# Optimization experiments

Measured on AMD Instinct MI355X. Metric: run time of the kernel, lower is better.

## Reference

```python
import jax, jax.numpy as jnp
import numpy as np

N_NODES = 100000
N_EDGES = 625000
D = 128


def setup_inputs() -> dict:
    key = jax.random.key(0)
    ks = jax.random.split(key, 6)
    x = jax.random.normal(ks[0], (N_NODES, D), dtype=jnp.float32)
    src = jax.random.randint(ks[1], (N_EDGES,), 0, N_NODES, dtype=jnp.int32)
    dst = jnp.sort(jax.random.randint(ks[2], (N_EDGES,), 0, N_NODES, dtype=jnp.int32))
    edge_w = jax.random.uniform(ks[3], (N_EDGES,), dtype=jnp.float32)
    # linear layer params (fan-in scaled)
    W = jax.random.normal(ks[4], (D, D), dtype=jnp.float32) / np.sqrt(D)
    b = jnp.zeros((D,), dtype=jnp.float32)
    # highway gate params (glorot-uniform-ish range as in source)
    init_range = np.sqrt(2.0 / (D + D)).astype(np.float32)
    kernel_gate = jax.random.uniform(ks[5], (D, D), dtype=jnp.float32,
                                     minval=-init_range, maxval=init_range)
    bias_gate = jnp.zeros((D,), dtype=jnp.float32)
    return {"x": x, "src": src, "dst": dst, "edge_w": edge_w,
            "W": W, "b": b, "kernel_gate": kernel_gate, "bias_gate": bias_gate}


def reference(x, src, dst, edge_w, W, b, kernel_gate, bias_gate):
    # hidden = Linear(x); dropout is identity in eval mode
    hidden = x @ W.T + b                                  # [N, D]
    # support = spmm(adj, hidden): gather src rows, weight, scatter-add to dst
    msgs = edge_w[:, None] * hidden[src]                  # [E, D]
    support = jax.ops.segment_sum(msgs, dst, num_segments=x.shape[0])
    support = jax.nn.relu(support)                        # act
    # highway gate
    gate = jax.nn.sigmoid(x @ kernel_gate + bias_gate)    # [N, D]
    out = gate * support + (1.0 - gate) * x
    return out
```

## Files before the change

kernel.cpp:

```cpp
#include <hip/hip_runtime.h>

#define DD 128

typedef __attribute__((ext_vector_type(8))) short bf16x8;
typedef __attribute__((ext_vector_type(4))) float f32x4;

__device__ __forceinline__ unsigned int cvt_pk_bf16(float lo, float hi) {
  unsigned int r;
  asm("v_cvt_pk_bf16_f32 %0, %1, %2" : "=v"(r) : "v"(lo), "v"(hi));
  return r;
}
__device__ __forceinline__ float bf_lo(unsigned int v) { return __uint_as_float(v << 16); }
__device__ __forceinline__ float bf_hi(unsigned int v) { return __uint_as_float(v & 0xFFFF0000u); }

__global__ void prep_kernel(const float* __restrict__ x, const int* __restrict__ dst,
                            const float* __restrict__ W, const float* __restrict__ KG,
                            unsigned short* __restrict__ xb, int* __restrict__ row_start,
                            unsigned short* __restrict__ B, int N, int E) {
  int i = blockIdx.x * 256 + threadIdx.x;
  int NC = N * (DD / 4);
  if (i < NC) {
    float4 v = ((const float4*)x)[i];
    uint2 q = {cvt_pk_bf16(v.x, v.y), cvt_pk_bf16(v.z, v.w)};
    ((uint2*)xb)[i] = q;
  } else if (i < NC + E + 1) {
    int e = i - NC;
    if (e == 0) {
      int d0 = dst[0];
      for (int n = 0; n <= d0; ++n) row_start[n] = 0;
    } else if (e == E) {
      for (int n = dst[E - 1] + 1; n <= N; ++n) row_start[n] = E;
    } else {
      int d = dst[e], dp = dst[e - 1];
      for (int n = dp + 1; n <= d; ++n) row_start[n] = e;
    }
  } else if (i < NC + E + 1 + 2 * DD * DD) {
    int e2 = i - (NC + E + 1);
    int j = e2 >> 7, k = e2 & 127;
    float v = (j < DD) ? W[j * DD + k] : KG[k * DD + (j - DD)];
    B[e2] = (unsigned short)cvt_pk_bf16(v, v);
  }
}

__global__ __launch_bounds__(256, 8) void scatter_agg(
    const unsigned short* __restrict__ xb, const int* __restrict__ src,
    const float* __restrict__ ew, const int* __restrict__ row_start,
    unsigned short* __restrict__ aggb, float* __restrict__ sumw, int N, int E) {
  int t = threadIdx.x;
  int wid = t >> 6, lane = t & 63;
  int q = lane >> 4, lr = lane & 15;
  int n = blockIdx.x * 16 + wid * 4 + q;
  bool valid = (n < N);
  int b = valid ? row_start[n] : 0;
  int cnt = valid ? (row_start[n + 1] - b) : 0;
  const uint4* x16 = (const uint4*)xb;

  float a[8];
#pragma unroll
  for (int k = 0; k < 8; ++k) a[k] = 0.f;
  float wsum = 0.f;
  int clampj = cnt > 0 ? cnt - 1 : 0;

  int i = 0;
  while (__any(i < cnt)) {
#pragma unroll
    for (int u = 0; u < 4; ++u) {
      int ii = i + u;
      int jj = ii < clampj ? ii : clampj;
      int j = b + jj;
      if (j > E - 1) j = E - 1;
      float wt = (ii < cnt) ? ew[j] : 0.f;
      int s = src[j];
      uint4 v = x16[(size_t)s * 16 + lr];
      wsum += wt;
      a[0] += wt * bf_lo(v.x); a[1] += wt * bf_hi(v.x);
      a[2] += wt * bf_lo(v.y); a[3] += wt * bf_hi(v.y);
      a[4] += wt * bf_lo(v.z); a[5] += wt * bf_hi(v.z);
      a[6] += wt * bf_lo(v.w); a[7] += wt * bf_hi(v.w);
    }
    i += 4;
  }

  if (valid) {
    uint4 o;
    o.x = cvt_pk_bf16(a[0], a[1]);
    o.y = cvt_pk_bf16(a[2], a[3]);
    o.z = cvt_pk_bf16(a[4], a[5]);
    o.w = cvt_pk_bf16(a[6], a[7]);
    ((uint4*)aggb)[(size_t)n * 16 + lr] = o;
    if (lr == 0) sumw[n] = wsum;
  }
}

__global__ __launch_bounds__(256, 2) void fused_gemm(
    const unsigned short* __restrict__ xb, const unsigned short* __restrict__ aggb,
    const unsigned short* __restrict__ B, const float* __restrict__ sumw,
    const float* __restrict__ bias, const float* __restrict__ bg,
    float* __restrict__ out, int N) {
  __shared__ char smem[32 * 1024];
  unsigned short* sX = (unsigned short*)smem;
  unsigned short* sA = (unsigned short*)(smem + 16384);
  int t = threadIdx.x;
  int wid = t >> 6, lane = t & 63;
  int lr = lane & 15, lk2 = lane >> 4;
  int jw = wid * 32;
  int M0 = blockIdx.x * 64;

  bf16x8 wS[4][2], wG[4][2];
#pragma unroll
  for (int kc = 0; kc < 4; ++kc)
#pragma unroll
    for (int m = 0; m < 2; ++m) {
      int j = jw + m * 16 + lr;
      wS[kc][m] = *(const bf16x8*)(B + (size_t)j * DD + kc * 32 + lk2 * 8);
      wG[kc][m] = *(const bf16x8*)(B + (size_t)(DD + j) * DD + kc * 32 + lk2 * 8);
    }
  float b4[2][4], bg4[2][4];
#pragma unroll
  for (int m = 0; m < 2; ++m) {
    *(float4*)b4[m]  = *(const float4*)&bias[jw + m * 16 + lk2 * 4];
    *(float4*)bg4[m] = *(const float4*)&bg[jw + m * 16 + lk2 * 4];
  }

#pragma unroll
  for (int i = 0; i < 4; ++i) {
    int idx = i * 256 + t;
    int r = idx >> 4, c = idx & 15;
    uint4 vx, va;
    if (M0 + r < N) {
      vx = ((const uint4*)(xb + (size_t)(M0 + r) * DD))[c];
      va = ((const uint4*)(aggb + (size_t)(M0 + r) * DD))[c];
    } else {
      vx = make_uint4(0, 0, 0, 0);
      va = make_uint4(0, 0, 0, 0);
    }
    int off = (r * 256 + c * 16) ^ ((r & 7) << 4);
    *(uint4*)((char*)sX + off) = vx;
    *(uint4*)((char*)sA + off) = va;
  }
  __syncthreads();

  f32x4 accS[2][4], accG[2][4];
#pragma unroll
  for (int m = 0; m < 2; ++m)
#pragma unroll
    for (int nr = 0; nr < 4; ++nr) {
      accS[m][nr] = (f32x4){0.f, 0.f, 0.f, 0.f};
      accG[m][nr] = (f32x4){0.f, 0.f, 0.f, 0.f};
    }

#pragma unroll
  for (int kc = 0; kc < 4; ++kc) {
    int kb = (kc * 32 + lk2 * 8) * 2;
    bf16x8 af[4], xf[4];
#pragma unroll
    for (int nr = 0; nr < 4; ++nr) {
      int r = nr * 16 + lr;
      int off = (r * 256 + kb) ^ ((r & 7) << 4);
      af[nr] = *(const bf16x8*)((const char*)sA + off);
      xf[nr] = *(const bf16x8*)((const char*)sX + off);
    }
#pragma unroll
    for (int m = 0; m < 2; ++m)
#pragma unroll
      for (int nr = 0; nr < 4; ++nr) {
        accS[m][nr] = __builtin_amdgcn_mfma_f32_16x16x32_bf16(wS[kc][m], af[nr], accS[m][nr], 0, 0, 0);
        accG[m][nr] = __builtin_amdgcn_mfma_f32_16x16x32_bf16(wG[kc][m], xf[nr], accG[m][nr], 0, 0, 0);
      }
  }

#pragma unroll
  for (int m = 0; m < 2; ++m) {
    int j0 = jw + m * 16 + lk2 * 4;
#pragma unroll
    for (int nr = 0; nr < 4; ++nr) {
      int node = M0 + nr * 16 + lr;
      if (node < N) {
        float sw = sumw[node];
        int r = nr * 16 + lr;
        uint2 qx = *(const uint2*)((const char*)sX + ((r * 256 + j0 * 2) ^ ((r & 7) << 4)));
        float xr[4] = {bf_lo(qx.x), bf_hi(qx.x), bf_lo(qx.y), bf_hi(qx.y)};
        f32x4 vs = accS[m][nr], vg = accG[m][nr];
        float4 o;
        float* op = &o.x;
#pragma unroll
        for (int reg = 0; reg < 4; ++reg) {
          float s = fmaxf(vs[reg] + sw * b4[m][reg], 0.f);
          float g = 1.0f / (1.0f + __expf(-(vg[reg] + bg4[m][reg])));
          op[reg] = g * s + (1.0f - g) * xr[reg];
        }
        *(float4*)&out[(size_t)node * DD + j0] = o;
      }
    }
  }
}

extern "C" void kernel_launch(void* const* d_in, const int* in_sizes, int n_in,
                              void* d_out, int out_size, void* d_ws, size_t ws_size,
                              hipStream_t stream) {
  const float* x   = (const float*)d_in[0];
  const int*   src = (const int*)d_in[1];
  const int*   dst = (const int*)d_in[2];
  const float* ew  = (const float*)d_in[3];
  const float* W   = (const float*)d_in[4];
  const float* b   = (const float*)d_in[5];
  const float* KG  = (const float*)d_in[6];
  const float* bg  = (const float*)d_in[7];
  float* out = (float*)d_out;

  int N = in_sizes[0] / DD;
  int E = in_sizes[1];

  unsigned short* xbuf = (unsigned short*)d_ws;
  unsigned short* aggb = xbuf + (size_t)N * DD;
  unsigned short* B    = aggb + (size_t)N * DD;
  float* sumw = (float*)(B + 2 * DD * DD);
  int* row_start = (int*)(sumw + N);

  int totalPrep = N * (DD / 4) + (E + 1) + 2 * DD * DD;
  prep_kernel<<<(totalPrep + 255) / 256, 256, 0, stream>>>(x, dst, W, KG, xbuf, row_start, B, N, E);
  scatter_agg<<<(N + 15) / 16, 256, 0, stream>>>(xbuf, src, ew, row_start, aggb, sumw, N, E);
  fused_gemm<<<(N + 63) / 64, 256, 0, stream>>>(xbuf, aggb, B, sumw, b, bg, out, N);
}
```

Baseline: 81.73 us.

## Fuse gather-aggregation into GEMM kernel via shared-memory staging

```diff
diff --git a/kernel.cpp b/kernel.cpp
--- a/kernel.cpp
+++ b/kernel.cpp
@@ -42,101 +42,87 @@
   }
 }
 
-__global__ __launch_bounds__(256, 8) void scatter_agg(
-    const unsigned short* __restrict__ xb, const int* __restrict__ src,
-    const float* __restrict__ ew, const int* __restrict__ row_start,
-    unsigned short* __restrict__ aggb, float* __restrict__ sumw, int N, int E) {
+__global__ __launch_bounds__(256, 2) void mega_kernel(
+    const unsigned short* __restrict__ xb, const unsigned short* __restrict__ B,
+    const int* __restrict__ src, const float* __restrict__ ew,
+    const int* __restrict__ row_start, const float* __restrict__ bias,
+    const float* __restrict__ bg, float* __restrict__ out, int N, int E) {
+  __shared__ char smem[32 * 1024 + 256];
+  unsigned short* sX = (unsigned short*)smem;
+  unsigned short* sA = (unsigned short*)(smem + 16384);
+  float* sumw_s = (float*)(smem + 32768);
   int t = threadIdx.x;
   int wid = t >> 6, lane = t & 63;
-  int q = lane >> 4, lr = lane & 15;
-  int n = blockIdx.x * 16 + wid * 4 + q;
-  bool valid = (n < N);
-  int b = valid ? row_start[n] : 0;
-  int cnt = valid ? (row_start[n + 1] - b) : 0;
+  int lr = lane & 15, lk2 = lane >> 4;
+  int jw = wid * 32;
+  int M0 = blockIdx.x * 64;
+
+  bf16x8 wS[4][2], wG[4][2];
+#pragma unroll
+  for (int kc = 0; kc < 4; ++kc)
+#pragma unroll
+    for (int m = 0; m < 2; ++m) {
+      int j = jw + m * 16 + lr;
+      wS[kc][m] = *(const bf16x8*)(B + (size_t)j * DD + kc * 32 + lk2 * 8);
+      wG[kc][m] = *(const bf16x8*)(B + (size_t)(DD + j) * DD + kc * 32 + lk2 * 8);
+    }
+  float b4[2][4], bg4[2][4];
+#pragma unroll
+  for (int m = 0; m < 2; ++m) {
+    *(float4*)b4[m]  = *(const float4*)&bias[jw + m * 16 + lk2 * 4];
+    *(float4*)bg4[m] = *(const float4*)&bg[jw + m * 16 + lk2 * 4];
+  }
+
+#pragma unroll
+  for (int i = 0; i < 4; ++i) {
+    int idx = i * 256 + t;
+    int r = idx >> 4, c = idx & 15;
+    uint4 vx;
+    if (M0 + r < N) vx = ((const uint4*)(xb + (size_t)(M0 + r) * DD))[c];
+    else            vx = make_uint4(0, 0, 0, 0);
+    int off = (r * 256 + c * 16) ^ ((r & 7) << 4);
+    *(uint4*)((char*)sX + off) = vx;
+  }
+
   const uint4* x16 = (const uint4*)xb;
-
-  float a[8];
-#pragma unroll
-  for (int k = 0; k < 8; ++k) a[k] = 0.f;
-  float wsum = 0.f;
-  int clampj = cnt > 0 ? cnt - 1 : 0;
-
-  int i = 0;
-  while (__any(i < cnt)) {
-#pragma unroll
-    for (int u = 0; u < 4; ++u) {
-      int ii = i + u;
-      int jj = ii < clampj ? ii : clampj;
-      int j = b + jj;
-      if (j > E - 1) j = E - 1;
-      float wt = (ii < cnt) ? ew[j] : 0.f;
-      int s = src[j];
-      uint4 v = x16[(size_t)s * 16 + lr];
-      wsum += wt;
-      a[0] += wt * bf_lo(v.x); a[1] += wt * bf_hi(v.x);
-      a[2] += wt * bf_lo(v.y); a[3] += wt * bf_hi(v.y);
-      a[4] += wt * bf_lo(v.z); a[5] += wt * bf_hi(v.z);
-      a[6] += wt * bf_lo(v.w); a[7] += wt * bf_hi(v.w);
-    }
-    i += 4;
-  }
-
-  if (valid) {
+  for (int p = 0; p < 4; ++p) {
+    int rt = wid * 16 + p * 4 + lk2;
+    int n = M0 + rt;
+    bool valid = (n < N);
+    int b = valid ? row_start[n] : 0;
+    int cnt = valid ? (row_start[n + 1] - b) : 0;
+    float a[8];
+#pragma unroll
+    for (int k = 0; k < 8; ++k) a[k] = 0.f;
+    float wsum = 0.f;
+    int clampj = cnt > 0 ? cnt - 1 : 0;
+    int i = 0;
+    while (__any(i < cnt)) {
+#pragma unroll
+      for (int u = 0; u < 4; ++u) {
+        int ii = i + u;
+        int jj = ii < clampj ? ii : clampj;
+        int j = b + jj;
+        if (j > E - 1) j = E - 1;
+        float wt = (ii < cnt) ? ew[j] : 0.f;
+        int s = src[j];
+        uint4 v = x16[(size_t)s * 16 + lr];
+        wsum += wt;
+        a[0] += wt * bf_lo(v.x); a[1] += wt * bf_hi(v.x);
+        a[2] += wt * bf_lo(v.y); a[3] += wt * bf_hi(v.y);
+        a[4] += wt * bf_lo(v.z); a[5] += wt * bf_hi(v.z);
+        a[6] += wt * bf_lo(v.w); a[7] += wt * bf_hi(v.w);
+      }
+      i += 4;
+    }
     uint4 o;
     o.x = cvt_pk_bf16(a[0], a[1]);
     o.y = cvt_pk_bf16(a[2], a[3]);
     o.z = cvt_pk_bf16(a[4], a[5]);
     o.w = cvt_pk_bf16(a[6], a[7]);
-    ((uint4*)aggb)[(size_t)n * 16 + lr] = o;
-    if (lr == 0) sumw[n] = wsum;
-  }
-}
-
-__global__ __launch_bounds__(256, 2) void fused_gemm(
-    const unsigned short* __restrict__ xb, const unsigned short* __restrict__ aggb,
-    const unsigned short* __restrict__ B, const float* __restrict__ sumw,
-    const float* __restrict__ bias, const float* __restrict__ bg,
-    float* __restrict__ out, int N) {
-  __shared__ char smem[32 * 1024];
-  unsigned short* sX = (unsigned short*)smem;
-  unsigned short* sA = (unsigned short*)(smem + 16384);
-  int t = threadIdx.x;
-  int wid = t >> 6, lane = t & 63;
-  int lr = lane & 15, lk2 = lane >> 4;
-  int jw = wid * 32;
-  int M0 = blockIdx.x * 64;
-
-  bf16x8 wS[4][2], wG[4][2];
-#pragma unroll
-  for (int kc = 0; kc < 4; ++kc)
-#pragma unroll
-    for (int m = 0; m < 2; ++m) {
-      int j = jw + m * 16 + lr;
-      wS[kc][m] = *(const bf16x8*)(B + (size_t)j * DD + kc * 32 + lk2 * 8);
-      wG[kc][m] = *(const bf16x8*)(B + (size_t)(DD + j) * DD + kc * 32 + lk2 * 8);
-    }
-  float b4[2][4], bg4[2][4];
-#pragma unroll
-  for (int m = 0; m < 2; ++m) {
-    *(float4*)b4[m]  = *(const float4*)&bias[jw + m * 16 + lk2 * 4];
-    *(float4*)bg4[m] = *(const float4*)&bg[jw + m * 16 + lk2 * 4];
-  }
-
-#pragma unroll
-  for (int i = 0; i < 4; ++i) {
-    int idx = i * 256 + t;
-    int r = idx >> 4, c = idx & 15;
-    uint4 vx, va;
-    if (M0 + r < N) {
-      vx = ((const uint4*)(xb + (size_t)(M0 + r) * DD))[c];
-      va = ((const uint4*)(aggb + (size_t)(M0 + r) * DD))[c];
-    } else {
-      vx = make_uint4(0, 0, 0, 0);
-      va = make_uint4(0, 0, 0, 0);
-    }
-    int off = (r * 256 + c * 16) ^ ((r & 7) << 4);
-    *(uint4*)((char*)sX + off) = vx;
-    *(uint4*)((char*)sA + off) = va;
+    int off = (rt * 256 + lr * 16) ^ ((rt & 7) << 4);
+    *(uint4*)((char*)sA + off) = o;
+    if (lr == 0) sumw_s[rt] = wsum;
   }
   __syncthreads();
 
@@ -176,8 +162,8 @@
     for (int nr = 0; nr < 4; ++nr) {
       int node = M0 + nr * 16 + lr;
       if (node < N) {
-        float sw = sumw[node];
         int r = nr * 16 + lr;
+        float sw = sumw_s[r];
         uint2 qx = *(const uint2*)((const char*)sX + ((r * 256 + j0 * 2) ^ ((r & 7) << 4)));
         float xr[4] = {bf_lo(qx.x), bf_hi(qx.x), bf_lo(qx.y), bf_hi(qx.y)};
         f32x4 vs = accS[m][nr], vg = accG[m][nr];
@@ -212,13 +198,10 @@
   int E = in_sizes[1];
 
   unsigned short* xbuf = (unsigned short*)d_ws;
-  unsigned short* aggb = xbuf + (size_t)N * DD;
-  unsigned short* B    = aggb + (size_t)N * DD;
-  float* sumw = (float*)(B + 2 * DD * DD);
-  int* row_start = (int*)(sumw + N);
+  unsigned short* B    = xbuf + (size_t)N * DD;
+  int* row_start = (int*)(B + 2 * DD * DD);
 
   int totalPrep = N * (DD / 4) + (E + 1) + 2 * DD * DD;
   prep_kernel<<<(totalPrep + 255) / 256, 256, 0, stream>>>(x, dst, W, KG, xbuf, row_start, B, N, E);
-  scatter_agg<<<(N + 15) / 16, 256, 0, stream>>>(xbuf, src, ew, row_start, aggb, sumw, N, E);
-  fused_gemm<<<(N + 63) / 64, 256, 0, stream>>>(xbuf, aggb, B, sumw, b, bg, out, N);
-}
+  mega_kernel<<<(N + 63) / 64, 256, 0, stream>>>(xbuf, B, src, ew, row_start, b, bg, out, N, E);
+}
```

Result: slower. 125.3 us (+53.3%).

## Quantize gathered node features to int8 with per-row scale for aggregation

Applied to the files above, without the earlier changes.

```diff
diff --git a/kernel.cpp b/kernel.cpp
--- a/kernel.cpp
+++ b/kernel.cpp
@@ -13,52 +13,87 @@
 __device__ __forceinline__ float bf_lo(unsigned int v) { return __uint_as_float(v << 16); }
 __device__ __forceinline__ float bf_hi(unsigned int v) { return __uint_as_float(v & 0xFFFF0000u); }
 
-__global__ void prep_kernel(const float* __restrict__ x, const int* __restrict__ dst,
-                            const float* __restrict__ W, const float* __restrict__ KG,
-                            unsigned short* __restrict__ xb, int* __restrict__ row_start,
-                            unsigned short* __restrict__ B, int N, int E) {
-  int i = blockIdx.x * 256 + threadIdx.x;
-  int NC = N * (DD / 4);
-  if (i < NC) {
-    float4 v = ((const float4*)x)[i];
-    uint2 q = {cvt_pk_bf16(v.x, v.y), cvt_pk_bf16(v.z, v.w)};
-    ((uint2*)xb)[i] = q;
-  } else if (i < NC + E + 1) {
-    int e = i - NC;
-    if (e == 0) {
-      int d0 = dst[0];
-      for (int n = 0; n <= d0; ++n) row_start[n] = 0;
-    } else if (e == E) {
-      for (int n = dst[E - 1] + 1; n <= N; ++n) row_start[n] = E;
-    } else {
-      int d = dst[e], dp = dst[e - 1];
-      for (int n = dp + 1; n <= d; ++n) row_start[n] = e;
-    }
-  } else if (i < NC + E + 1 + 2 * DD * DD) {
-    int e2 = i - (NC + E + 1);
-    int j = e2 >> 7, k = e2 & 127;
-    float v = (j < DD) ? W[j * DD + k] : KG[k * DD + (j - DD)];
-    B[e2] = (unsigned short)cvt_pk_bf16(v, v);
+__global__ __launch_bounds__(256) void prep_kernel(
+    const float* __restrict__ x, const int* __restrict__ dst,
+    const float* __restrict__ W, const float* __restrict__ KG,
+    unsigned short* __restrict__ xb, unsigned char* __restrict__ xq,
+    float* __restrict__ sx, int* __restrict__ row_start,
+    unsigned short* __restrict__ B, int N, int E, int ABLK, int BBLK) {
+  int blk = blockIdx.x;
+  int t = threadIdx.x;
+  if (blk < ABLK) {
+    int n = blk * 16 + (t >> 4);
+    int lr = t & 15;
+    if (n < N) {
+      const float4* xr = (const float4*)(x + (size_t)n * DD);
+      float4 va = xr[lr * 2], vb = xr[lr * 2 + 1];
+      float m = fmaxf(fmaxf(fmaxf(fabsf(va.x), fabsf(va.y)), fmaxf(fabsf(va.z), fabsf(va.w))),
+                      fmaxf(fmaxf(fabsf(vb.x), fabsf(vb.y)), fmaxf(fabsf(vb.z), fabsf(vb.w))));
+#pragma unroll
+      for (int d = 1; d < 16; d <<= 1) m = fmaxf(m, __shfl_xor(m, d, 16));
+      m = fmaxf(m, 1e-20f);
+      float inv = 127.0f / m;
+      unsigned int q0 = (unsigned int)(__float2int_rn(va.x * inv) + 128);
+      unsigned int q1 = (unsigned int)(__float2int_rn(va.y * inv) + 128);
+      unsigned int q2 = (unsigned int)(__float2int_rn(va.z * inv) + 128);
+      unsigned int q3 = (unsigned int)(__float2int_rn(va.w * inv) + 128);
+      unsigned int q4 = (unsigned int)(__float2int_rn(vb.x * inv) + 128);
+      unsigned int q5 = (unsigned int)(__float2int_rn(vb.y * inv) + 128);
+      unsigned int q6 = (unsigned int)(__float2int_rn(vb.z * inv) + 128);
+      unsigned int q7 = (unsigned int)(__float2int_rn(vb.w * inv) + 128);
+      uint2 qp;
+      qp.x = q0 | (q1 << 8) | (q2 << 16) | (q3 << 24);
+      qp.y = q4 | (q5 << 8) | (q6 << 16) | (q7 << 24);
+      ((uint2*)xq)[(size_t)n * 16 + lr] = qp;
+      uint4 bp;
+      bp.x = cvt_pk_bf16(va.x, va.y);
+      bp.y = cvt_pk_bf16(va.z, va.w);
+      bp.z = cvt_pk_bf16(vb.x, vb.y);
+      bp.w = cvt_pk_bf16(vb.z, vb.w);
+      ((uint4*)xb)[(size_t)n * 16 + lr] = bp;
+      if (lr == 0) sx[n] = m * (1.0f / 127.0f);
+    }
+  } else if (blk < ABLK + BBLK) {
+    int e = (blk - ABLK) * 256 + t;
+    if (e <= E) {
+      if (e == 0) {
+        int d0 = dst[0];
+        for (int n = 0; n <= d0; ++n) row_start[n] = 0;
+      } else if (e == E) {
+        for (int n = dst[E - 1] + 1; n <= N; ++n) row_start[n] = E;
+      } else {
+        int d = dst[e], dp = dst[e - 1];
+        for (int n = dp + 1; n <= d; ++n) row_start[n] = e;
+      }
+    }
+  } else {
+    int e2 = (blk - ABLK - BBLK) * 256 + t;
+    if (e2 < 2 * DD * DD) {
+      int j = e2 >> 7, k = e2 & 127;
+      float v = (j < DD) ? W[j * DD + k] : KG[k * DD + (j - DD)];
+      B[e2] = (unsigned short)cvt_pk_bf16(v, v);
+    }
   }
 }
 
 __global__ __launch_bounds__(256, 8) void scatter_agg(
-    const unsigned short* __restrict__ xb, const int* __restrict__ src,
-    const float* __restrict__ ew, const int* __restrict__ row_start,
-    unsigned short* __restrict__ aggb, float* __restrict__ sumw, int N, int E) {
+    const unsigned char* __restrict__ xq, const float* __restrict__ sx,
+    const int* __restrict__ src, const float* __restrict__ ew,
+    const int* __restrict__ row_start, unsigned short* __restrict__ aggb,
+    float* __restrict__ sumw, int N, int E) {
   int t = threadIdx.x;
   int wid = t >> 6, lane = t & 63;
-  int q = lane >> 4, lr = lane & 15;
-  int n = blockIdx.x * 16 + wid * 4 + q;
+  int g = lane >> 4, lr = lane & 15;
+  int n = blockIdx.x * 16 + wid * 4 + g;
   bool valid = (n < N);
   int b = valid ? row_start[n] : 0;
   int cnt = valid ? (row_start[n + 1] - b) : 0;
-  const uint4* x16 = (const uint4*)xb;
+  const uint2* x8 = (const uint2*)xq;
 
   float a[8];
 #pragma unroll
   for (int k = 0; k < 8; ++k) a[k] = 0.f;
-  float wsum = 0.f;
+  float wsum = 0.f, wsc = 0.f;
   int clampj = cnt > 0 ? cnt - 1 : 0;
 
   int i = 0;
@@ -71,15 +106,24 @@
       if (j > E - 1) j = E - 1;
       float wt = (ii < cnt) ? ew[j] : 0.f;
       int s = src[j];
-      uint4 v = x16[(size_t)s * 16 + lr];
+      float ws = wt * sx[s];
+      uint2 v = x8[(size_t)s * 16 + lr];
       wsum += wt;
-      a[0] += wt * bf_lo(v.x); a[1] += wt * bf_hi(v.x);
-      a[2] += wt * bf_lo(v.y); a[3] += wt * bf_hi(v.y);
-      a[4] += wt * bf_lo(v.z); a[5] += wt * bf_hi(v.z);
-      a[6] += wt * bf_lo(v.w); a[7] += wt * bf_hi(v.w);
+      wsc += ws;
+      a[0] += ws * (float)(v.x & 0xFF);
+      a[1] += ws * (float)((v.x >> 8) & 0xFF);
+      a[2] += ws * (float)((v.x >> 16) & 0xFF);
+      a[3] += ws * (float)(v.x >> 24);
+      a[4] += ws * (float)(v.y & 0xFF);
+      a[5] += ws * (float)((v.y >> 8) & 0xFF);
+      a[6] += ws * (float)((v.y >> 16) & 0xFF);
+      a[7] += ws * (float)(v.y >> 24);
     }
     i += 4;
   }
+  float c = 128.0f * wsc;
+#pragma unroll
+  for (int k = 0; k < 8; ++k) a[k] -= c;
 
   if (valid) {
     uint4 o;
@@ -92,7 +136,7 @@
   }
 }
 
-__global__ __launch_bounds__(256, 2) void fused_gemm(
+__global__ __launch_bounds__(256, 4) void fused_gemm(
     const unsigned short* __restrict__ xb, const unsigned short* __restrict__ aggb,
     const unsigned short* __restrict__ B, const float* __restrict__ sumw,
     const float* __restrict__ bias, const float* __restrict__ bg,
@@ -106,22 +150,6 @@
   int jw = wid * 32;
   int M0 = blockIdx.x * 64;
 
-  bf16x8 wS[4][2], wG[4][2];
-#pragma unroll
-  for (int kc = 0; kc < 4; ++kc)
-#pragma unroll
-    for (int m = 0; m < 2; ++m) {
-      int j = jw + m * 16 + lr;
-      wS[kc][m] = *(const bf16x8*)(B + (size_t)j * DD + kc * 32 + lk2 * 8);
-      wG[kc][m] = *(const bf16x8*)(B + (size_t)(DD + j) * DD + kc * 32 + lk2 * 8);
-    }
-  float b4[2][4], bg4[2][4];
-#pragma unroll
-  for (int m = 0; m < 2; ++m) {
-    *(float4*)b4[m]  = *(const float4*)&bias[jw + m * 16 + lk2 * 4];
-    *(float4*)bg4[m] = *(const float4*)&bg[jw + m * 16 + lk2 * 4];
-  }
-
 #pragma unroll
   for (int i = 0; i < 4; ++i) {
     int idx = i * 256 + t;
@@ -152,6 +180,13 @@
 #pragma unroll
   for (int kc = 0; kc < 4; ++kc) {
     int kb = (kc * 32 + lk2 * 8) * 2;
+    bf16x8 wSk[2], wGk[2];
+#pragma unroll
+    for (int m = 0; m < 2; ++m) {
+      int j = jw + m * 16 + lr;
+      wSk[m] = *(const bf16x8*)(B + (size_t)j * DD + kc * 32 + lk2 * 8);
+      wGk[m] = *(const bf16x8*)(B + (size_t)(DD + j) * DD + kc * 32 + lk2 * 8);
+    }
     bf16x8 af[4], xf[4];
 #pragma unroll
     for (int nr = 0; nr < 4; ++nr) {
@@ -164,14 +199,18 @@
     for (int m = 0; m < 2; ++m)
 #pragma unroll
       for (int nr = 0; nr < 4; ++nr) {
-        accS[m][nr] = __builtin_amdgcn_mfma_f32_16x16x32_bf16(wS[kc][m], af[nr], accS[m][nr], 0, 0, 0);
-        accG[m][nr] = __builtin_amdgcn_mfma_f32_16x16x32_bf16(wG[kc][m], xf[nr], accG[m][nr], 0, 0, 0);
+        accS[m][nr] = __builtin_amdgcn_mfma_f32_16x16x32_bf16(wSk[m], af[nr], accS[m][nr], 0, 0, 0);
+        accG[m][nr] = __builtin_amdgcn_mfma_f32_16x16x32_bf16(wGk[m], xf[nr], accG[m][nr], 0, 0, 0);
       }
   }
 
 #pragma unroll
   for (int m = 0; m < 2; ++m) {
     int j0 = jw + m * 16 + lk2 * 4;
+    float4 b4 = *(const float4*)&bias[j0];
+    float4 bg4 = *(const float4*)&bg[j0];
+    float ba[4] = {b4.x, b4.y, b4.z, b4.w};
+    float bga[4] = {bg4.x, bg4.y, bg4.z, bg4.w};
 #pragma unroll
     for (int nr = 0; nr < 4; ++nr) {
       int node = M0 + nr * 16 + lr;
@@ -185,8 +224,8 @@
         float* op = &o.x;
 #pragma unroll
         for (int reg = 0; reg < 4; ++reg) {
-          float s = fmaxf(vs[reg] + sw * b4[m][reg], 0.f);
-          float g = 1.0f / (1.0f + __expf(-(vg[reg] + bg4[m][reg])));
+          float s = fmaxf(vs[reg] + sw * ba[reg], 0.f);
+          float g = 1.0f / (1.0f + __expf(-(vg[reg] + bga[reg])));
           op[reg] = g * s + (1.0f - g) * xr[reg];
         }
         *(float4*)&out[(size_t)node * DD + j0] = o;
@@ -211,14 +250,19 @@
   int N = in_sizes[0] / DD;
   int E = in_sizes[1];
 
-  unsigned short* xbuf = (unsigned short*)d_ws;
-  unsigned short* aggb = xbuf + (size_t)N * DD;
-  unsigned short* B    = aggb + (size_t)N * DD;
-  float* sumw = (float*)(B + 2 * DD * DD);
-  int* row_start = (int*)(sumw + N);
-
-  int totalPrep = N * (DD / 4) + (E + 1) + 2 * DD * DD;
-  prep_kernel<<<(totalPrep + 255) / 256, 256, 0, stream>>>(x, dst, W, KG, xbuf, row_start, B, N, E);
-  scatter_agg<<<(N + 15) / 16, 256, 0, stream>>>(xbuf, src, ew, row_start, aggb, sumw, N, E);
-  fused_gemm<<<(N + 63) / 64, 256, 0, stream>>>(xbuf, aggb, B, sumw, b, bg, out, N);
-}
+  unsigned short* xb = (unsigned short*)d_ws;
+  unsigned short* aggb = xb + (size_t)N * DD;
+  unsigned char* xq = (unsigned char*)(aggb + (size_t)N * DD);
+  float* sx = (float*)(xq + (size_t)N * DD);
+  float* sumw = sx + N;
+  unsigned short* B = (unsigned short*)(sumw + N);
+  int* row_start = (int*)(B + 2 * DD * DD);
+
+  int ABLK = (N + 15) / 16;
+  int BBLK = (E + 1 + 255) / 256;
+  int CBLK = (2 * DD * DD + 255) / 256;
+  prep_kernel<<<ABLK + BBLK + CBLK, 256, 0, stream>>>(x, dst, W, KG, xb, xq, sx,
+                                                      row_start, B, N, E, ABLK, BBLK);
+  scatter_agg<<<(N + 15) / 16, 256, 0, stream>>>(xq, sx, src, ew, row_start, aggb, sumw, N, E);
+  fused_gemm<<<(N + 63) / 64, 256, 0, stream>>>(xb, aggb, B, sumw, b, bg, out, N);
+}
```

After: 80.90 us. No clear change (-1.0%).
